# Performance work log

Hardware: AMD Instinct MI355X
Metric: run time of the kernel (lower is better)

The kernel has to match this reference:

```python
import jax, jax.numpy as jnp
import numpy as np

TARGET_MAIN_CONTRIBUTION = 0.6
CONTRIB_LOSS_COEF = 0.01
TOP_K = 2
NEG_INF = -1e9


def _gat(x, adj, W1, a1s, a1d, W2, a2s, a2d):
    """Dense 2-layer GAT (pyGAT style): multi-head concat + ELU, then one output head.
    x: [B,S,Fin], adj: [B,S,S], W1: [H,Fin,Fh], a1s/a1d: [H,Fh], W2: [H*Fh,Fout], a2s/a2d: [Fout]."""
    mask = adj > 0  # [B,S,S]
    h = jnp.einsum('bsf,hfo->bhso', x, W1)                      # [B,H,S,Fh]
    es = jnp.einsum('bhso,ho->bhs', h, a1s)
    ed = jnp.einsum('bhso,ho->bhs', h, a1d)
    e = jax.nn.leaky_relu(es[:, :, :, None] + ed[:, :, None, :], 0.2)  # [B,H,S,S]
    att = jax.nn.softmax(jnp.where(mask[:, None], e, NEG_INF), axis=-1)
    h1 = jax.nn.elu(jnp.einsum('bhst,bhto->bhso', att, h))      # [B,H,S,Fh]
    B, H, S, Fh = h1.shape
    h1 = h1.transpose(0, 2, 1, 3).reshape(B, S, H * Fh)         # concat heads
    h2 = h1 @ W2                                                # [B,S,Fout]
    e2 = jax.nn.leaky_relu((h2 @ a2s)[:, :, None] + (h2 @ a2d)[:, None, :], 0.2)
    att2 = jax.nn.softmax(jnp.where(mask, e2, NEG_INF), axis=-1)
    return jnp.einsum('bst,bto->bso', att2, h2)


def setup_inputs() -> dict:
    B, S, D, H, Hd, E = 4, 1024, 256, 6, 64, 3
    key = jax.random.key(0)
    ks = jax.random.split(key, 20)
    feature = jax.random.normal(ks[0], (B, S, D), dtype=jnp.float32)
    # sparse-ish binary adjacency with self-loops
    adj = (jax.random.uniform(ks[1], (B, S, S)) < 0.05).astype(jnp.float32)
    adj = jnp.maximum(adj, jnp.eye(S, dtype=jnp.float32)[None])
    p = lambda k, shape: jax.random.normal(k, shape, dtype=jnp.float32) * 0.1
    return {
        'feature': feature, 'adj': adj,
        'main_W1': p(ks[2], (H, D, Hd)), 'main_a1s': p(ks[3], (H, Hd)), 'main_a1d': p(ks[4], (H, Hd)),
        'main_W2': p(ks[5], (H * Hd, D)), 'main_a2s': p(ks[6], (D,)), 'main_a2d': p(ks[7], (D,)),
        'dep_W1': p(ks[8], (E, H, D, Hd)), 'dep_a1s': p(ks[9], (E, H, Hd)), 'dep_a1d': p(ks[10], (E, H, Hd)),
        'dep_W2': p(ks[11], (E, H * Hd, D)), 'dep_a2s': p(ks[12], (E, D)), 'dep_a2d': p(ks[13], (E, D)),
        'router_W': p(ks[14], (D, E)),
        'blend_W': p(ks[15], (D, D)), 'blend_b': jnp.zeros((D,), dtype=jnp.float32),
        'doc_num': 4, 'sect_num': 32,
    }


def reference(feature, adj, main_W1, main_a1s, main_a1d, main_W2, main_a2s, main_a2d,
              dep_W1, dep_a1s, dep_a1d, dep_W2, dep_a2s, dep_a2d,
              router_W, blend_W, blend_b, doc_num, sect_num):
    B, S, D = feature.shape
    E = router_W.shape[1]
    # main expert on full graph
    main_output = _gat(feature, adj, main_W1, main_a1s, main_a1d, main_W2, main_a2s, main_a2d)
    # per-expert adjacency views (zero out columns by node type)
    col = jnp.arange(S)
    sent_cols = (col < S - sect_num - doc_num).astype(adj.dtype)
    sect_cols = ((col >= S - sect_num - doc_num) & (col < S - doc_num)).astype(adj.dtype)
    doc_cols = (col >= S - doc_num).astype(adj.dtype)
    adj_stack = jnp.stack([adj * sent_cols, adj * sect_cols, adj * doc_cols])  # [E,B,S,S]
    # fixed top-k router
    x_flat = feature.reshape(-1, D)
    gate_probs = jax.nn.softmax(x_flat @ router_W, axis=-1)      # [B*S,E]
    _, top_idx = jax.lax.top_k(gate_probs, TOP_K)                # [B*S,k]
    routing_mask = jax.nn.one_hot(top_idx, E, dtype=feature.dtype).sum(axis=-2)  # [B*S,E] binary
    routing_mask = routing_mask.reshape(B, S, E)
    mask_e = routing_mask.transpose(2, 0, 1)[..., None]          # [E,B,S,1]
    # deputy experts: masked input, masked output, accumulate
    x_e = feature[None] * mask_e                                 # [E,B,S,D]
    dep_out = jax.vmap(_gat)(x_e, adj_stack, dep_W1, dep_a1s, dep_a1d, dep_W2, dep_a2s, dep_a2d)
    deputy_output = (dep_out * mask_e).sum(axis=0)               # [B,S,D]
    # blend gate
    blend_weight = jax.nn.sigmoid(feature @ blend_W + blend_b)
    final_output = blend_weight * main_output + (1.0 - blend_weight) * deputy_output
    main_contribution = blend_weight.mean()
    contribution_loss = jnp.abs(main_contribution - TARGET_MAIN_CONTRIBUTION) * CONTRIB_LOSS_COEF
    return final_output, contribution_loss, main_contribution
```

## Files before the change

kernel.cpp:

```cpp
#include <hip/hip_runtime.h>
#include <math.h>

#define B 4
#define S 1024
#define D 256
#define H 6
#define HD 64
#define NE 3
#define HHD 384
#define ROWS (B*S)
#define MAXN 128

typedef __attribute__((ext_vector_type(8))) short bf8_t;
typedef __attribute__((ext_vector_type(4))) float f32x4;

__device__ __forceinline__ float leaky(float x){ return x > 0.f ? x : 0.2f*x; }

__device__ __forceinline__ unsigned short f2bf(float f){
    union { float f; unsigned int u; } v; v.f = f;
    unsigned int u = v.u;
    return (unsigned short)((u + 0x7FFFu + ((u >> 16) & 1u)) >> 16);
}
__device__ __forceinline__ float bf2f(unsigned short h){
    union { unsigned int u; float f; } v; v.u = ((unsigned int)h) << 16;
    return v.f;
}
__device__ __forceinline__ float blo(unsigned int u){
    union { unsigned int u; float f; } v; v.u = u << 16; return v.f;
}
__device__ __forceinline__ float bhi(unsigned int u){
    union { unsigned int u; float f; } v; v.u = u & 0xffff0000u; return v.f;
}
__device__ __forceinline__ float i2f(int t){
    union { int i; float f; } v; v.i = t; return v.f;
}
__device__ __forceinline__ int f2i(float f){
    union { float f; int i; } v; v.f = f; return v.i;
}
__device__ __forceinline__ unsigned int pk2(float lo, float hi){
    return (unsigned)f2bf(lo) | ((unsigned)f2bf(hi) << 16);
}

struct P {
    const float *feature, *adj;
    const float *main_W1, *dep_W1, *main_W2, *dep_W2, *blend_W, *router_W;
    const int *doc_p, *sect_p;
    const float *main_a1s, *main_a1d, *dep_a1s, *dep_a1d;
    const float *main_a2s, *main_a2d, *dep_a2s, *dep_a2d;
    const float *blend_b;
    unsigned short *featbf; short *nbr; int4 *nbc;
    unsigned short *w1nk, *w2nk, *bwt;
    float *es8, *ed8, *gatebuf;
    unsigned short *htn4, *h2n4, *h1c4;
    float *f2s4, *f2d4, *meanV1p, *meanV2, *sumBuf, *rmask;
    float *outp;
};

#define PB_CONV   1024
#define PB_NBR    1024
#define PB_W1     1536
#define PB_W2     1536
#define PB_BW      256
#define PB_ZERO    177
#define PB_ROUTER 1024
#define PB_TOTAL  (PB_CONV + PB_NBR + PB_W1 + PB_W2 + PB_BW + PB_ZERO + PB_ROUTER)
#define NZERO     45088

__global__ __launch_bounds__(256) void prep_kernel(P pp)
{
    int blk = blockIdx.x, tid = threadIdx.x;
    if (blk < PB_CONV){
        int idx = blk*256 + tid;
        float4 v = ((const float4*)pp.feature)[idx];
        ushort4 o;
        o.x = f2bf(v.x); o.y = f2bf(v.y); o.z = f2bf(v.z); o.w = f2bf(v.w);
        ((ushort4*)pp.featbf)[idx] = o;
        return;
    }
    blk -= PB_CONV;
    if (blk < PB_NBR){
        int wave = tid >> 6, lane = tid & 63;
        int row = blk*4 + wave;
        int b1 = S - *pp.sect_p - *pp.doc_p;
        int b2 = S - *pp.doc_p;
        const float* ar = pp.adj + (size_t)row*S + lane*16;
        float a[16];
        #pragma unroll
        for (int q = 0; q < 4; q++){
            float4 v = ((const float4*)ar)[q];
            a[q*4+0] = v.x; a[q*4+1] = v.y; a[q*4+2] = v.z; a[q*4+3] = v.w;
        }
        int t0 = lane*16;
        int k = 0, c1 = 0, c2 = 0;
        #pragma unroll
        for (int i = 0; i < 16; i++){
            if (a[i] > 0.f){
                k++;
                int t = t0 + i;
                if (t < b1) c1++;
                if (t < b2) c2++;
            }
        }
        int inc = k;
        #pragma unroll
        for (int d = 1; d < 64; d <<= 1){
            int u = __shfl_up(inc, d);
            if (lane >= d) inc += u;
        }
        int off = inc - k;
        int total = __shfl(inc, 63);
        int o = row*MAXN + off;
        #pragma unroll
        for (int i = 0; i < 16; i++){
            if (a[i] > 0.f) pp.nbr[o++] = (short)(t0 + i);
        }
        for (int d = 32; d; d >>= 1){
            c1 += __shfl_down(c1, d);
            c2 += __shfl_down(c2, d);
        }
        if (lane == 0) pp.nbc[row] = make_int4(total, c1, c2, 0);
        return;
    }
    blk -= PB_NBR;
    if (blk < PB_W1){
        int e = blk / 384;
        int idx = (blk - e*384)*256 + tid;
        const float* src = (e == 0) ? pp.main_W1 : pp.dep_W1 + (size_t)(e-1)*H*D*HD;
        int n = idx >> 8, k = idx & 255;
        int h = n >> 6, o = n & 63;
        pp.w1nk[(size_t)e*HHD*D + idx] = f2bf(src[(h*D + k)*HD + o]);
        return;
    }
    blk -= PB_W1;
    if (blk < PB_W2){
        int g = blk*256 + tid;
        int e = g / (D*HHD);
        int rem = g - e*(D*HHD);
        int n = rem / HHD, k = rem - n*HHD;
        const float* src = (e == 0) ? pp.main_W2 : pp.dep_W2 + (size_t)(e-1)*HHD*D;
        pp.w2nk[g] = f2bf(src[k*D + n]);
        return;
    }
    blk -= PB_W2;
    if (blk < PB_BW){
        int col = blk, k = tid;
        pp.bwt[col*D + k] = f2bf(pp.blend_W[k*D + col]);
        return;
    }
    blk -= PB_BW;
    if (blk < PB_ZERO){
        int idx = blk*256 + tid;
        if (idx < NZERO) pp.f2s4[idx] = 0.f;
        return;
    }
    blk -= PB_ZERO;
    {
        int wave = tid >> 6, lane = tid & 63;
        int row = blk*4 + wave;
        float4 xv = ((const float4*)(pp.feature + (size_t)row*D))[lane];
        int f = lane*4;
        float xa[4] = {xv.x, xv.y, xv.z, xv.w};
        float p0 = 0.f, p1 = 0.f, p2 = 0.f;
        #pragma unroll
        for (int j = 0; j < 4; j++){
            p0 += xa[j]*pp.router_W[(f+j)*NE + 0];
            p1 += xa[j]*pp.router_W[(f+j)*NE + 1];
            p2 += xa[j]*pp.router_W[(f+j)*NE + 2];
        }
        for (int off = 32; off; off >>= 1){
            p0 += __shfl_down(p0, off);
            p1 += __shfl_down(p1, off);
            p2 += __shfl_down(p2, off);
        }
        if (lane == 0){
            float p[3] = {p0, p1, p2};
            int ex = 0;
            for (int e = 1; e < NE; e++) if (p[e] <= p[ex]) ex = e;
            for (int e = 0; e < NE; e++) pp.rmask[e*ROWS + row] = (e == ex) ? 0.f : 1.f;
        }
    }
}

__global__ __launch_bounds__(256, 4) void gemm1_kernel(P pp)
{
    __shared__ float ep[2][2][64][17];
    int tid = threadIdx.x, wave = tid >> 6, lane = tid & 63;
    int quad = lane >> 4, l16 = lane & 15;
    int e = blockIdx.z;
    int n0 = blockIdx.y*64;
    f32x4 z4 = {0.f,0.f,0.f,0.f};
    bf8_t bz = {0,0,0,0,0,0,0,0};

    if (e == 4){
        if (blockIdx.x >= 2) return;
        int m0 = blockIdx.x*128;
        const unsigned short* arow0 = pp.bwt + (size_t)(m0 + wave*16 + l16)*D + quad*8;
        const unsigned short* arow1 = arow0 + (size_t)64*D;
        const unsigned short* brow[4];
        #pragma unroll
        for (int j = 0; j < 4; j++)
            brow[j] = pp.featbf + (size_t)(n0 + j*16 + l16)*D + quad*8;
        f32x4 acc[8] = {z4, z4, z4, z4, z4, z4, z4, z4};
        bf8_t a0F = *(const bf8_t*)(arow0);
        bf8_t a1F = *(const bf8_t*)(arow1);
        bf8_t bF[4];
        #pragma unroll
        for (int j = 0; j < 4; j++) bF[j] = *(const bf8_t*)(brow[j]);
        #pragma unroll
        for (int it = 0; it < D/32; it++){
            bf8_t a0C = a0F, a1C = a1F;
            bf8_t bC[4] = {bF[0], bF[1], bF[2], bF[3]};
            if (it + 1 < D/32){
                int kn = (it + 1)*32;
                a0F = *(const bf8_t*)(arow0 + kn);
                a1F = *(const bf8_t*)(arow1 + kn);
                #pragma unroll
                for (int j = 0; j < 4; j++) bF[j] = *(const bf8_t*)(brow[j] + kn);
            }
            #pragma unroll
            for (int j = 0; j < 4; j++){
                acc[j]   = __builtin_amdgcn_mfma_f32_16x16x32_bf16(a0C, bC[j], acc[j],   0, 0, 0);
                acc[4+j] = __builtin_amdgcn_mfma_f32_16x16x32_bf16(a1C, bC[j], acc[4+j], 0, 0, 0);
            }
        }
        int mbase0 = m0 + wave*16 + quad*4;
        int mbase1 = mbase0 + 64;
        float bias0[4], bias1[4];
        #pragma unroll
        for (int r = 0; r < 4; r++){ bias0[r] = pp.blend_b[mbase0 + r]; bias1[r] = pp.blend_b[mbase1 + r]; }
        float lsum = 0.f;
        #pragma unroll
        for (int j = 0; j < 4; j++){
            int rown = n0 + j*16 + l16;
            f32x4 st0, st1;
            #pragma unroll
            for (int r = 0; r < 4; r++){
                float g0 = 1.f/(1.f + __expf(-(acc[j][r] + bias0[r])));
                float g1 = 1.f/(1.f + __expf(-(acc[4+j][r] + bias1[r])));
                lsum += g0 + g1;
                st0[r] = g0; st1[r] = g1;
            }
            *(f32x4*)(pp.gatebuf + (size_t)rown*D + mbase0) = st0;
            *(f32x4*)(pp.gatebuf + (size_t)rown*D + mbase1) = st1;
        }
        float* redp = &ep[0][0][0][0];
        redp[tid] = lsum;
        __syncthreads();
        for (int sft = 128; sft; sft >>= 1){
            if (tid < sft) redp[tid] += redp[tid + sft];
            __syncthreads();
        }
        if (tid == 0) atomicAdd(pp.sumBuf, redp[0]);
        return;
    }

    int p = blockIdx.x;
    int m0 = p*128;
    const unsigned short* arow0 = pp.w1nk + (size_t)e*HHD*D + (size_t)(m0 + wave*16 + l16)*D + quad*8;
    const unsigned short* arow1 = arow0 + (size_t)64*D;
    const unsigned short* brow[4];
    bool zr[4];
    #pragma unroll
    for (int j = 0; j < 4; j++){
        int n = n0 + j*16 + l16;
        brow[j] = pp.featbf + (size_t)n*D + quad*8;
        zr[j] = (e > 0) ? (pp.rmask[(size_t)(e-1)*ROWS + n] == 0.f) : false;
    }
    f32x4 acc[8] = {z4, z4, z4, z4, z4, z4, z4, z4};
    bf8_t a0F = *(const bf8_t*)(arow0);
    bf8_t a1F = *(const bf8_t*)(arow1);
    bf8_t bF[4];
    #pragma unroll
    for (int j = 0; j < 4; j++) bF[j] = zr[j] ? bz : *(const bf8_t*)(brow[j]);
    #pragma unroll
    for (int it = 0; it < D/32; it++){
        bf8_t a0C = a0F, a1C = a1F;
        bf8_t bC[4] = {bF[0], bF[1], bF[2], bF[3]};
        if (it + 1 < D/32){
            int kn = (it + 1)*32;
            a0F = *(const bf8_t*)(arow0 + kn);
            a1F = *(const bf8_t*)(arow1 + kn);
            #pragma unroll
            for (int j = 0; j < 4; j++) bF[j] = zr[j] ? bz : *(const bf8_t*)(brow[j] + kn);
        }
        #pragma unroll
        for (int j = 0; j < 4; j++){
            acc[j]   = __builtin_amdgcn_mfma_f32_16x16x32_bf16(a0C, bC[j], acc[j],   0, 0, 0);
            acc[4+j] = __builtin_amdgcn_mfma_f32_16x16x32_bf16(a1C, bC[j], acc[4+j], 0, 0, 0);
        }
    }
    int b = n0 >> 10;
    int mbase0 = m0 + wave*16 + quad*4;
    int mbase1 = mbase0 + 64;
    int obase = wave*16 + quad*4;
    int h0 = p*2, h1 = p*2 + 1;
    unsigned int* hp4 = (unsigned int*)pp.htn4;
    #pragma unroll
    for (int j = 0; j < 4; j++){
        int row = n0 + j*16 + l16;
        unsigned int* dst = hp4 + ((size_t)e*ROWS + row)*256 + obase*4 + p;
        dst[0]  = pk2(acc[j][0], acc[4+j][0]);
        dst[4]  = pk2(acc[j][1], acc[4+j][1]);
        dst[8]  = pk2(acc[j][2], acc[4+j][2]);
        dst[12] = pk2(acc[j][3], acc[4+j][3]);
    }
    const float* a1sp = (e == 0) ? pp.main_a1s : pp.dep_a1s + (size_t)(e-1)*H*HD;
    const float* a1dp = (e == 0) ? pp.main_a1d : pp.dep_a1d + (size_t)(e-1)*H*HD;
    float s0v[4], d0v[4], s1v[4], d1v[4];
    #pragma unroll
    for (int r = 0; r < 4; r++){
        s0v[r] = a1sp[mbase0 + r]; d0v[r] = a1dp[mbase0 + r];
        s1v[r] = a1sp[mbase1 + r]; d1v[r] = a1dp[mbase1 + r];
    }
    #pragma unroll
    for (int j = 0; j < 4; j++){
        float ps0 = 0.f, pd0 = 0.f, ps1 = 0.f, pd1 = 0.f;
        #pragma unroll
        for (int r = 0; r < 4; r++){
            ps0 += acc[j][r]*s0v[r];   pd0 += acc[j][r]*d0v[r];
            ps1 += acc[4+j][r]*s1v[r]; pd1 += acc[4+j][r]*d1v[r];
        }
        ep[0][0][j*16 + l16][wave*4 + quad] = ps0;
        ep[0][1][j*16 + l16][wave*4 + quad] = pd0;
        ep[1][0][j*16 + l16][wave*4 + quad] = ps1;
        ep[1][1][j*16 + l16][wave*4 + quad] = pd1;
    }
    float* mvb = pp.meanV1p + ((size_t)e*B + b)*512;
    #pragma unroll
    for (int r = 0; r < 4; r++){
        float cm0 = acc[0][r] + acc[1][r] + acc[2][r] + acc[3][r];
        float cm1 = acc[4][r] + acc[5][r] + acc[6][r] + acc[7][r];
        for (int off = 8; off; off >>= 1){
            cm0 += __shfl_down(cm0, off, 16);
            cm1 += __shfl_down(cm1, off, 16);
        }
        if (l16 == 0){
            atomicAdd(mvb + (obase + r)*8 + h0, cm0*(1.f/(float)S));
            atomicAdd(mvb + (obase + r)*8 + h1, cm1*(1.f/(float)S));
        }
    }
    __syncthreads();
    {
        int hh = tid >> 7, arr = (tid >> 6) & 1, sl = tid & 63;
        float sum = 0.f;
        #pragma unroll
        for (int i = 0; i < 16; i++) sum += ep[hh][arr][sl][i];
        int n = n0 + sl;
        float* dst = arr ? pp.ed8 : pp.es8;
        dst[(((size_t)e*B + (n >> 10))*S + (n & 1023))*8 + (p*2 + hh)] = sum;
    }
}

__global__ __launch_bounds__(256) void a1_kernel(P pp)
{
    __shared__ f32x4 wMa[MAXN], wMb[MAXN], wDa[MAXN], wDb[MAXN];
    __shared__ f32x4 paccA[4][64], paccB[4][64];
    __shared__ float pdenM[2][6];
    __shared__ float pdenD[2][3][6];
    int tid = threadIdx.x, wave = tid >> 6, lane = tid & 63;
    int s = blockIdx.x, b = blockIdx.y;
    int row = b*S + s;
    int4 c = pp.nbc[row];
    const short* nl = pp.nbr + (size_t)row*MAXN;

    if (wave < 2){
        const float* esp = pp.es8 + ((size_t)b*S + s)*8;
        f32x4 eslo = *(const f32x4*)esp;
        f32x4 eshi = *(const f32x4*)(esp + 4);
        float esv[6] = {eslo[0], eslo[1], eslo[2], eslo[3], eshi[0], eshi[1]};
        const float* edb = pp.ed8 + (size_t)b*S*8;
        int i = wave*64 + lane;
        float w[6] = {0,0,0,0,0,0};
        if (i < c.x){
            int t = nl[i];
            const float* epn = edb + (size_t)t*8;
            f32x4 d0 = *(const f32x4*)epn;
            f32x4 d1 = *(const f32x4*)(epn + 4);
            float edv[6] = {d0[0], d0[1], d0[2], d0[3], d1[0], d1[1]};
            #pragma unroll
            for (int h = 0; h < 6; h++) w[h] = __expf(leaky(esv[h] + edv[h]));
            f32x4 ra = {w[0], w[1], w[2], w[3]};
            f32x4 rb = {w[4], w[5], i2f(t), 0.f};
            wMa[i] = ra; wMb[i] = rb;
        }
        #pragma unroll
        for (int h = 0; h < 6; h++){
            float x = w[h];
            for (int o2 = 32; o2; o2 >>= 1) x += __shfl_down(x, o2);
            if (lane == 0) pdenM[wave][h] = x;
        }
    } else {
        int i = (wave - 2)*64 + lane;
        int tg = (i < c.y) ? 1 : ((i < c.z) ? 2 : 3);
        float w[6] = {0,0,0,0,0,0};
        if (i < c.x){
            int t = nl[i];
            const float* esp = pp.es8 + (((size_t)tg*B + b)*S + s)*8;
            f32x4 eslo = *(const f32x4*)esp;
            f32x4 eshi = *(const f32x4*)(esp + 4);
            const float* epn = pp.ed8 + (((size_t)tg*B + b)*S + (size_t)t)*8;
            f32x4 d0 = *(const f32x4*)epn;
            f32x4 d1 = *(const f32x4*)(epn + 4);
            float es6[6] = {eslo[0], eslo[1], eslo[2], eslo[3], eshi[0], eshi[1]};
            float ed6[6] = {d0[0], d0[1], d0[2], d0[3], d1[0], d1[1]};
            #pragma unroll
            for (int h = 0; h < 6; h++) w[h] = __expf(leaky(es6[h] + ed6[h]));
            float zf = (pp.rmask[(size_t)(tg-1)*ROWS + (size_t)b*S + t] == 0.f) ? 1.f : 0.f;
            f32x4 ra = {w[0], w[1], w[2], w[3]};
            f32x4 rb = {w[4], w[5], zf, 0.f};
            wDa[i] = ra; wDb[i] = rb;
        }
        #pragma unroll
        for (int g = 1; g <= 3; g++){
            #pragma unroll
            for (int h = 0; h < 6; h++){
                float x = (tg == g) ? w[h] : 0.f;
                for (int o2 = 32; o2; o2 >>= 1) x += __shfl_down(x, o2);
                if (lane == 0) pdenD[wave-2][g-1][h] = x;
            }
        }
    }
    __syncthreads();

    const unsigned int* V0 = (const unsigned int*)pp.htn4 + (size_t)b*S*256;
    float accM[6] = {0,0,0,0,0,0};
    int rlo[3] = {0, c.y, c.z};
    int rhi[3] = {c.y, c.z, c.x};
    for (int rg = 0; rg < 3; rg++){
        const unsigned int* Ve = (const unsigned int*)pp.htn4 + ((size_t)(rg+1)*ROWS + (size_t)b*S)*256;
        float accD[6] = {0,0,0,0,0,0};
        #pragma unroll 2
        for (int j = rlo[rg] + wave; j < rhi[rg]; j += 4){
            f32x4 ma = wMa[j], mb = wMb[j];
            f32x4 da = wDa[j], db = wDb[j];
            int t = f2i(mb[2]);
            uint4 vm = *(const uint4*)(V0 + ((size_t)t*64 + lane)*4);
            accM[0] += ma[0]*blo(vm.x); accM[1] += ma[1]*bhi(vm.x);
            accM[2] += ma[2]*blo(vm.y); accM[3] += ma[3]*bhi(vm.y);
            accM[4] += mb[0]*blo(vm.z); accM[5] += mb[1]*bhi(vm.z);
            if (db[2] == 0.f){
                uint4 vd = *(const uint4*)(Ve + ((size_t)t*64 + lane)*4);
                accD[0] += da[0]*blo(vd.x); accD[1] += da[1]*bhi(vd.x);
                accD[2] += da[2]*blo(vd.y); accD[3] += da[3]*bhi(vd.y);
                accD[4] += db[0]*blo(vd.z); accD[5] += db[1]*bhi(vd.z);
            }
        }
        {
            f32x4 pa = {accD[0], accD[1], accD[2], accD[3]};
            f32x4 pb = {accD[4], accD[5], 0.f, 0.f};
            paccA[wave][lane] = pa; paccB[wave][lane] = pb;
        }
        __syncthreads();
        if (wave == 0){
            unsigned short* outp = pp.h1c4 + ((size_t)(rg+1)*ROWS + row)*HHD;
            bool has = rhi[rg] > rlo[rg];
            const float* mv = pp.meanV1p + ((size_t)(rg+1)*B + b)*512 + lane*8;
            f32x4 q0 = paccA[0][lane], q1 = paccA[1][lane], q2 = paccA[2][lane], q3 = paccA[3][lane];
            f32x4 r0 = paccB[0][lane], r1 = paccB[1][lane], r2 = paccB[2][lane], r3 = paccB[3][lane];
            float sum6[6];
            sum6[0] = q0[0]+q1[0]+q2[0]+q3[0];
            sum6[1] = q0[1]+q1[1]+q2[1]+q3[1];
            sum6[2] = q0[2]+q1[2]+q2[2]+q3[2];
            sum6[3] = q0[3]+q1[3]+q2[3]+q3[3];
            sum6[4] = r0[0]+r1[0]+r2[0]+r3[0];
            sum6[5] = r0[1]+r1[1]+r2[1]+r3[1];
            #pragma unroll
            for (int h = 0; h < 6; h++){
                float den = pdenD[0][rg][h] + pdenD[1][rg][h];
                float v = has ? sum6[h]/den : mv[h];
                v = v > 0.f ? v : __expf(v) - 1.f;
                outp[h*64 + lane] = f2bf(v);
            }
        }
        __syncthreads();
    }
    {
        f32x4 pa = {accM[0], accM[1], accM[2], accM[3]};
        f32x4 pb = {accM[4], accM[5], 0.f, 0.f};
        paccA[wave][lane] = pa; paccB[wave][lane] = pb;
    }
    __syncthreads();
    if (wave == 0){
        unsigned short* outp = pp.h1c4 + (size_t)row*HHD;
        f32x4 q0 = paccA[0][lane], q1 = paccA[1][lane], q2 = paccA[2][lane], q3 = paccA[3][lane];
        f32x4 r0 = paccB[0][lane], r1 = paccB[1][lane], r2 = paccB[2][lane], r3 = paccB[3][lane];
        float sum6[6];
        sum6[0] = q0[0]+q1[0]+q2[0]+q3[0];
        sum6[1] = q0[1]+q1[1]+q2[1]+q3[1];
        sum6[2] = q0[2]+q1[2]+q2[2]+q3[2];
        sum6[3] = q0[3]+q1[3]+q2[3]+q3[3];
        sum6[4] = r0[0]+r1[0]+r2[0]+r3[0];
        sum6[5] = r0[1]+r1[1]+r2[1]+r3[1];
        #pragma unroll
        for (int h = 0; h < 6; h++){
            float den = pdenM[0][h] + pdenM[1][h];
            float v = sum6[h]/den;
            v = v > 0.f ? v : __expf(v) - 1.f;
            outp[h*64 + lane] = f2bf(v);
        }
    }
}

__global__ __launch_bounds__(256, 4) void gemm2_kernel(P pp)
{
    __shared__ float ep[2][2][64][17];
    int tid = threadIdx.x, wave = tid >> 6, lane = tid & 63;
    int quad = lane >> 4, l16 = lane & 15;
    int e = blockIdx.z;
    int m0 = blockIdx.x*128;
    int n0 = blockIdx.y*64;
    f32x4 z4 = {0.f,0.f,0.f,0.f};
    const unsigned short* arow0 = pp.w2nk + (size_t)e*D*HHD + (size_t)(m0 + wave*16 + l16)*HHD + quad*8;
    const unsigned short* arow1 = arow0 + (size_t)64*HHD;
    const unsigned short* brow[4];
    #pragma unroll
    for (int j = 0; j < 4; j++)
        brow[j] = pp.h1c4 + (size_t)e*ROWS*HHD + (size_t)(n0 + j*16 + l16)*HHD + quad*8;
    f32x4 acc[8] = {z4, z4, z4, z4, z4, z4, z4, z4};
    bf8_t a0F = *(const bf8_t*)(arow0);
    bf8_t a1F = *(const bf8_t*)(arow1);
    bf8_t bF[4];
    #pragma unroll
    for (int j = 0; j < 4; j++) bF[j] = *(const bf8_t*)(brow[j]);
    #pragma unroll
    for (int it = 0; it < HHD/32; it++){
        bf8_t a0C = a0F, a1C = a1F;
        bf8_t bC[4] = {bF[0], bF[1], bF[2], bF[3]};
        if (it + 1 < HHD/32){
            int kn = (it + 1)*32;
            a0F = *(const bf8_t*)(arow0 + kn);
            a1F = *(const bf8_t*)(arow1 + kn);
            #pragma unroll
            for (int j = 0; j < 4; j++) bF[j] = *(const bf8_t*)(brow[j] + kn);
        }
        #pragma unroll
        for (int j = 0; j < 4; j++){
            acc[j]   = __builtin_amdgcn_mfma_f32_16x16x32_bf16(a0C, bC[j], acc[j],   0, 0, 0);
            acc[4+j] = __builtin_amdgcn_mfma_f32_16x16x32_bf16(a1C, bC[j], acc[4+j], 0, 0, 0);
        }
    }
    int b = n0 >> 10;
    int mbase0 = m0 + wave*16 + quad*4;
    int mbase1 = mbase0 + 64;
    #pragma unroll
    for (int j = 0; j < 4; j++){
        int row = n0 + j*16 + l16;
        ushort4 o0, o1;
        o0.x = f2bf(acc[j][0]);   o0.y = f2bf(acc[j][1]);
        o0.z = f2bf(acc[j][2]);   o0.w = f2bf(acc[j][3]);
        o1.x = f2bf(acc[4+j][0]); o1.y = f2bf(acc[4+j][1]);
        o1.z = f2bf(acc[4+j][2]); o1.w = f2bf(acc[4+j][3]);
        *(ushort4*)(pp.h2n4 + ((size_t)e*ROWS + row)*D + mbase0) = o0;
        *(ushort4*)(pp.h2n4 + ((size_t)e*ROWS + row)*D + mbase1) = o1;
    }
    const float* a2sp = (e == 0) ? pp.main_a2s : pp.dep_a2s + (size_t)(e-1)*D;
    const float* a2dp = (e == 0) ? pp.main_a2d : pp.dep_a2d + (size_t)(e-1)*D;
    float s0v[4], d0v[4], s1v[4], d1v[4];
    #pragma unroll
    for (int r = 0; r < 4; r++){
        s0v[r] = a2sp[mbase0 + r]; d0v[r] = a2dp[mbase0 + r];
        s1v[r] = a2sp[mbase1 + r]; d1v[r] = a2dp[mbase1 + r];
    }
    #pragma unroll
    for (int j = 0; j < 4; j++){
        float ps0 = 0.f, pd0 = 0.f, ps1 = 0.f, pd1 = 0.f;
        #pragma unroll
        for (int r = 0; r < 4; r++){
            ps0 += acc[j][r]*s0v[r];   pd0 += acc[j][r]*d0v[r];
            ps1 += acc[4+j][r]*s1v[r]; pd1 += acc[4+j][r]*d1v[r];
        }
        ep[0][0][j*16 + l16][wave*4 + quad] = ps0;
        ep[0][1][j*16 + l16][wave*4 + quad] = pd0;
        ep[1][0][j*16 + l16][wave*4 + quad] = ps1;
        ep[1][1][j*16 + l16][wave*4 + quad] = pd1;
    }
    #pragma unroll
    for (int r = 0; r < 4; r++){
        float cm0 = acc[0][r] + acc[1][r] + acc[2][r] + acc[3][r];
        float cm1 = acc[4][r] + acc[5][r] + acc[6][r] + acc[7][r];
        for (int off = 8; off; off >>= 1){
            cm0 += __shfl_down(cm0, off, 16);
            cm1 += __shfl_down(cm1, off, 16);
        }
        if (l16 == 0){
            atomicAdd(pp.meanV2 + ((size_t)e*B + b)*D + mbase0 + r, cm0*(1.f/(float)S));
            atomicAdd(pp.meanV2 + ((size_t)e*B + b)*D + mbase1 + r, cm1*(1.f/(float)S));
        }
    }
    __syncthreads();
    {
        int hh = tid >> 7, arr = (tid >> 6) & 1, sl = tid & 63;
        float sum = 0.f;
        #pragma unroll
        for (int i = 0; i < 16; i++) sum += ep[hh][arr][sl][i];
        int n = n0 + sl;
        float* dst = arr ? pp.f2d4 : pp.f2s4;
        atomicAdd(dst + (size_t)e*ROWS + n, sum);
    }
}

__global__ __launch_bounds__(256) void a2_kernel(P pp)
{
    __shared__ float2 wrec0[MAXN];
    __shared__ float2 wrec1[MAXN];
    __shared__ float pacc[3][256];
    __shared__ float pden[4][4];
    int tid = threadIdx.x;
    int wave = tid >> 6, lane = tid & 63;
    int s = blockIdx.x, b = blockIdx.y;
    int row = b*S + s;
    int4 c = pp.nbc[row];
    float rm0 = pp.rmask[row], rm1 = pp.rmask[ROWS + row], rm2 = pp.rmask[2*ROWS + row];
    const short* nl = pp.nbr + (size_t)row*MAXN;
    if (wave < 2){
        int i = wave*64 + lane;
        float w = 0.f;
        if (i < c.x){
            int t = nl[i];
            float fs = pp.f2s4[row];
            w = __expf(leaky(fs + pp.f2d4[(size_t)b*S + t]));
            float2 r; r.x = w; r.y = i2f(t);
            wrec0[i] = r;
        }
        float dsum = w;
        for (int o2 = 32; o2; o2 >>= 1) dsum += __shfl_down(dsum, o2);
        if (lane == 0) pden[wave][0] = dsum;
    } else {
        int i = (wave - 2)*64 + lane;
        float w = 0.f, d1 = 0.f, d2 = 0.f, d3 = 0.f;
        if (i < c.x){
            int t = nl[i];
            int tag = (i < c.y) ? 1 : ((i < c.z) ? 2 : 3);
            float act = (tag == 1) ? rm0 : ((tag == 2) ? rm1 : rm2);
            if (act != 0.f){
                float fs = pp.f2s4[(size_t)tag*ROWS + row];
                w = __expf(leaky(fs + pp.f2d4[(size_t)tag*ROWS + (size_t)b*S + t]));
            }
            float2 r; r.x = w; r.y = i2f(t);
            wrec1[i] = r;
            if (tag == 1) d1 = w; else if (tag == 2) d2 = w; else d3 = w;
        }
        for (int o2 = 32; o2; o2 >>= 1){
            d1 += __shfl_down(d1, o2);
            d2 += __shfl_down(d2, o2);
            d3 += __shfl_down(d3, o2);
        }
        if (lane == 0){ pden[wave][1] = d1; pden[wave][2] = d2; pden[wave][3] = d3; }
    }
    __syncthreads();
    float acc[4] = {0.f, 0.f, 0.f, 0.f};
    if (wave < 2){
        float inv = 1.f/(pden[0][0] + pden[1][0]);
        const unsigned short* V = pp.h2n4 + (size_t)b*S*D;
        #pragma unroll 4
        for (int j = wave; j < c.x; j += 2){
            float2 r = wrec0[j];
            float wv = r.x*inv;
            int t = f2i(r.y);
            const unsigned short* vp = V + (size_t)t*D + lane*4;
            uint2 dv = *(const uint2*)vp;
            acc[0] += wv*blo(dv.x); acc[1] += wv*bhi(dv.x);
            acc[2] += wv*blo(dv.y); acc[3] += wv*bhi(dv.y);
        }
    } else {
        int rlo[3] = {0, c.y, c.z};
        int rhi[3] = {c.y, c.z, c.x};
        float ract[3] = {rm0, rm1, rm2};
        for (int rg = 0; rg < 3; rg++){
            if (ract[rg] == 0.f || rhi[rg] <= rlo[rg]) continue;
            float inv = 1.f/(pden[2][rg+1] + pden[3][rg+1]);
            const unsigned short* V = pp.h2n4 + ((size_t)(rg+1)*ROWS + (size_t)b*S)*D;
            #pragma unroll 4
            for (int j = rlo[rg] + (wave - 2); j < rhi[rg]; j += 2){
                float2 r = wrec1[j];
                float wv = r.x*inv;
                int t = f2i(r.y);
                const unsigned short* vp = V + (size_t)t*D + lane*4;
                uint2 dv = *(const uint2*)vp;
                acc[0] += wv*blo(dv.x); acc[1] += wv*bhi(dv.x);
                acc[2] += wv*blo(dv.y); acc[3] += wv*bhi(dv.y);
            }
        }
    }
    if (wave >= 1){
        #pragma unroll
        for (int q = 0; q < 4; q++) pacc[wave-1][lane*4 + q] = acc[q];
    }
    __syncthreads();
    if (wave == 0){
        float4 g4 = *(const float4*)(pp.gatebuf + (size_t)row*D + lane*4);
        float dep_mv[4] = {0.f, 0.f, 0.f, 0.f};
        if (rm0 != 0.f && c.y == 0){
            float4 mv = *(const float4*)(pp.meanV2 + ((size_t)1*B + b)*D + lane*4);
            dep_mv[0] += mv.x; dep_mv[1] += mv.y; dep_mv[2] += mv.z; dep_mv[3] += mv.w;
        }
        if (rm1 != 0.f && c.z == c.y){
            float4 mv = *(const float4*)(pp.meanV2 + ((size_t)2*B + b)*D + lane*4);
            dep_mv[0] += mv.x; dep_mv[1] += mv.y; dep_mv[2] += mv.z; dep_mv[3] += mv.w;
        }
        if (rm2 != 0.f && c.x == c.z){
            float4 mv = *(const float4*)(pp.meanV2 + ((size_t)3*B + b)*D + lane*4);
            dep_mv[0] += mv.x; dep_mv[1] += mv.y; dep_mv[2] += mv.z; dep_mv[3] += mv.w;
        }
        float g[4] = {g4.x, g4.y, g4.z, g4.w};
        float4 o;
        float* op = &o.x;
        #pragma unroll
        for (int q = 0; q < 4; q++){
            int col = lane*4 + q;
            float a0 = acc[q] + pacc[0][col];
            float dep = pacc[1][col] + pacc[2][col] + dep_mv[q];
            op[q] = g[q]*a0 + (1.f - g[q])*dep;
        }
        *(float4*)(pp.outp + (size_t)row*D + lane*4) = o;
    }
    if (blockIdx.x == 0 && blockIdx.y == 0 && tid == 0){
        float mc = pp.sumBuf[0] / (float)(ROWS*D);
        pp.outp[ROWS*D]     = fabsf(mc - 0.6f)*0.01f;
        pp.outp[ROWS*D + 1] = mc;
    }
}

extern "C" void kernel_launch(void* const* d_in, const int* in_sizes, int n_in,
                              void* d_out, int out_size, void* d_ws, size_t ws_size,
                              hipStream_t stream)
{
    P hp;
    hp.feature  = (const float*)d_in[0];
    hp.adj      = (const float*)d_in[1];
    hp.main_W1  = (const float*)d_in[2];
    hp.main_a1s = (const float*)d_in[3];
    hp.main_a1d = (const float*)d_in[4];
    hp.main_W2  = (const float*)d_in[5];
    hp.main_a2s = (const float*)d_in[6];
    hp.main_a2d = (const float*)d_in[7];
    hp.dep_W1   = (const float*)d_in[8];
    hp.dep_a1s  = (const float*)d_in[9];
    hp.dep_a1d  = (const float*)d_in[10];
    hp.dep_W2   = (const float*)d_in[11];
    hp.dep_a2s  = (const float*)d_in[12];
    hp.dep_a2d  = (const float*)d_in[13];
    hp.router_W = (const float*)d_in[14];
    hp.blend_W  = (const float*)d_in[15];
    hp.blend_b  = (const float*)d_in[16];
    hp.doc_p    = (const int*)d_in[17];
    hp.sect_p   = (const int*)d_in[18];

    char* ws = (char*)d_ws;
    size_t off = 0;
    hp.featbf = (unsigned short*)(ws + off); off += (size_t)ROWS*D*2;
    hp.nbr    = (short*)(ws + off);          off += (size_t)ROWS*MAXN*2;
    hp.nbc    = (int4*)(ws + off);           off += (size_t)ROWS*16;
    hp.w1nk   = (unsigned short*)(ws + off); off += (size_t)4*HHD*D*2;
    hp.w2nk   = (unsigned short*)(ws + off); off += (size_t)4*D*HHD*2;
    hp.bwt    = (unsigned short*)(ws + off); off += (size_t)D*D*2;
    hp.es8 = (float*)(ws + off); off += (size_t)4*B*S*8*4;
    hp.ed8 = (float*)(ws + off); off += (size_t)4*B*S*8*4;
    hp.gatebuf = (float*)(ws + off); off += (size_t)ROWS*D*4;
    hp.htn4 = (unsigned short*)(ws + off); off += (size_t)4*ROWS*256*4;
    hp.h2n4 = (unsigned short*)(ws + off); off += (size_t)4*ROWS*D*2;
    hp.h1c4 = (unsigned short*)(ws + off); off += (size_t)4*ROWS*HHD*2;
    hp.f2s4    = (float*)(ws + off); off += (size_t)4*ROWS*4;
    hp.f2d4    = (float*)(ws + off); off += (size_t)4*ROWS*4;
    hp.meanV1p = (float*)(ws + off); off += (size_t)4*B*512*4;
    hp.meanV2  = (float*)(ws + off); off += (size_t)4*B*D*4;
    hp.sumBuf  = (float*)(ws + off); off += 128;
    hp.rmask   = (float*)(ws + off); off += (size_t)NE*ROWS*4;
    hp.outp    = (float*)d_out;

    prep_kernel<<<PB_TOTAL, 256, 0, stream>>>(hp);
    gemm1_kernel<<<dim3(3, ROWS/64, 5), 256, 0, stream>>>(hp);
    a1_kernel<<<dim3(S, B), 256, 0, stream>>>(hp);
    gemm2_kernel<<<dim3(D/128, ROWS/64, 4), 256, 0, stream>>>(hp);
    a2_kernel<<<dim3(S, B), 256, 0, stream>>>(hp);
}
```

Baseline: 226.0 us.

## Store layer-1 head features as per-pair planes via LDS-staged coalesced writes

The interleaved htn4 buffer, which held 4 uint slots per output with one unused, is replaced by three separate planes per expert, one per head pair. gemm1 now stages the packed bf16 results in shared memory and writes each plane with coalesced 16-byte stores. The a1 gather now reads three 4-byte words from separate planes instead of one 16-byte word. This drops the wasted padding slot and the strided scatter stores, but each gathered neighbour now costs three memory transactions instead of one.

Result: faster. 221.5 us (-2.0%).

```diff
diff --git a/kernel.cpp b/kernel.cpp
--- a/kernel.cpp
+++ b/kernel.cpp
@@ -10,6 +10,7 @@
 #define HHD 384
 #define ROWS (B*S)
 #define MAXN 128
+#define PLN ((size_t)ROWS*64)
 
 typedef __attribute__((ext_vector_type(8))) short bf8_t;
 typedef __attribute__((ext_vector_type(4))) float f32x4;
@@ -51,7 +52,8 @@
     unsigned short *featbf; short *nbr; int4 *nbc;
     unsigned short *w1nk, *w2nk, *bwt;
     float *es8, *ed8, *gatebuf;
-    unsigned short *htn4, *h2n4, *h1c4;
+    unsigned int *htp;
+    unsigned short *h2n4, *h1c4;
     float *f2s4, *f2d4, *meanV1p, *meanV2, *sumBuf, *rmask;
     float *outp;
 };
@@ -183,7 +185,9 @@
 
 __global__ __launch_bounds__(256, 4) void gemm1_kernel(P pp)
 {
-    __shared__ float ep[2][2][64][17];
+    __shared__ __align__(16) char smem[17408];
+    float (*ep)[2][64][17] = (float (*)[2][64][17])smem;
+    unsigned int (*tile)[68] = (unsigned int (*)[68])smem;
     int tid = threadIdx.x, wave = tid >> 6, lane = tid & 63;
     int quad = lane >> 4, l16 = lane & 15;
     int e = blockIdx.z;
@@ -243,7 +247,7 @@
             *(f32x4*)(pp.gatebuf + (size_t)rown*D + mbase0) = st0;
             *(f32x4*)(pp.gatebuf + (size_t)rown*D + mbase1) = st1;
         }
-        float* redp = &ep[0][0][0][0];
+        float* redp = (float*)smem;
         redp[tid] = lsum;
         __syncthreads();
         for (int sft = 128; sft; sft >>= 1){
@@ -294,16 +298,6 @@
     int mbase1 = mbase0 + 64;
     int obase = wave*16 + quad*4;
     int h0 = p*2, h1 = p*2 + 1;
-    unsigned int* hp4 = (unsigned int*)pp.htn4;
-    #pragma unroll
-    for (int j = 0; j < 4; j++){
-        int row = n0 + j*16 + l16;
-        unsigned int* dst = hp4 + ((size_t)e*ROWS + row)*256 + obase*4 + p;
-        dst[0]  = pk2(acc[j][0], acc[4+j][0]);
-        dst[4]  = pk2(acc[j][1], acc[4+j][1]);
-        dst[8]  = pk2(acc[j][2], acc[4+j][2]);
-        dst[12] = pk2(acc[j][3], acc[4+j][3]);
-    }
     const float* a1sp = (e == 0) ? pp.main_a1s : pp.dep_a1s + (size_t)(e-1)*H*HD;
     const float* a1dp = (e == 0) ? pp.main_a1d : pp.dep_a1d + (size_t)(e-1)*H*HD;
     float s0v[4], d0v[4], s1v[4], d1v[4];
@@ -348,6 +342,27 @@
         int n = n0 + sl;
         float* dst = arr ? pp.ed8 : pp.es8;
         dst[(((size_t)e*B + (n >> 10))*S + (n & 1023))*8 + (p*2 + hh)] = sum;
+    }
+    __syncthreads();
+    #pragma unroll
+    for (int j = 0; j < 4; j++){
+        int rloc = j*16 + l16;
+        tile[rloc][obase + 0] = pk2(acc[j][0], acc[4+j][0]);
+        tile[rloc][obase + 1] = pk2(acc[j][1], acc[4+j][1]);
+        tile[rloc][obase + 2] = pk2(acc[j][2], acc[4+j][2]);
+        tile[rloc][obase + 3] = pk2(acc[j][3], acc[4+j][3]);
+    }
+    __syncthreads();
+    {
+        unsigned int* plane = pp.htp + (size_t)(e*3 + p)*PLN;
+        int o4 = (tid & 15)*4;
+        int rsub = tid >> 4;
+        #pragma unroll
+        for (int pass = 0; pass < 4; pass++){
+            int rloc = pass*16 + rsub;
+            uint4 v = *(const uint4*)&tile[rloc][o4];
+            *(uint4*)(plane + (size_t)(n0 + rloc)*64 + o4) = v;
+        }
     }
 }
 
@@ -422,27 +437,31 @@
     }
     __syncthreads();
 
-    const unsigned int* V0 = (const unsigned int*)pp.htn4 + (size_t)b*S*256;
+    const unsigned int* Vm = pp.htp + (size_t)b*S*64 + lane;
     float accM[6] = {0,0,0,0,0,0};
     int rlo[3] = {0, c.y, c.z};
     int rhi[3] = {c.y, c.z, c.x};
     for (int rg = 0; rg < 3; rg++){
-        const unsigned int* Ve = (const unsigned int*)pp.htn4 + ((size_t)(rg+1)*ROWS + (size_t)b*S)*256;
+        const unsigned int* Vd = pp.htp + (size_t)(rg+1)*3*PLN + (size_t)b*S*64 + lane;
         float accD[6] = {0,0,0,0,0,0};
         #pragma unroll 2
         for (int j = rlo[rg] + wave; j < rhi[rg]; j += 4){
             f32x4 ma = wMa[j], mb = wMb[j];
             f32x4 da = wDa[j], db = wDb[j];
-            int t = f2i(mb[2]);
-            uint4 vm = *(const uint4*)(V0 + ((size_t)t*64 + lane)*4);
-            accM[0] += ma[0]*blo(vm.x); accM[1] += ma[1]*bhi(vm.x);
-            accM[2] += ma[2]*blo(vm.y); accM[3] += ma[3]*bhi(vm.y);
-            accM[4] += mb[0]*blo(vm.z); accM[5] += mb[1]*bhi(vm.z);
+            size_t toff = (size_t)f2i(mb[2])*64;
+            unsigned int u0 = Vm[toff];
+            unsigned int u1 = Vm[toff + PLN];
+            unsigned int u2 = Vm[toff + 2*PLN];
+            accM[0] += ma[0]*blo(u0); accM[1] += ma[1]*bhi(u0);
+            accM[2] += ma[2]*blo(u1); accM[3] += ma[3]*bhi(u1);
+            accM[4] += mb[0]*blo(u2); accM[5] += mb[1]*bhi(u2);
             if (db[2] == 0.f){
-                uint4 vd = *(const uint4*)(Ve + ((size_t)t*64 + lane)*4);
-                accD[0] += da[0]*blo(vd.x); accD[1] += da[1]*bhi(vd.x);
-                accD[2] += da[2]*blo(vd.y); accD[3] += da[3]*bhi(vd.y);
-                accD[4] += db[0]*blo(vd.z); accD[5] += db[1]*bhi(vd.z);
+                unsigned int d0 = Vd[toff];
+                unsigned int d1 = Vd[toff + PLN];
+                unsigned int d2 = Vd[toff + 2*PLN];
+                accD[0] += da[0]*blo(d0); accD[1] += da[1]*bhi(d0);
+                accD[2] += da[2]*blo(d1); accD[3] += da[3]*bhi(d1);
+                accD[4] += db[0]*blo(d2); accD[5] += db[1]*bhi(d2);
             }
         }
         {
@@ -757,7 +776,7 @@
     hp.es8 = (float*)(ws + off); off += (size_t)4*B*S*8*4;
     hp.ed8 = (float*)(ws + off); off += (size_t)4*B*S*8*4;
     hp.gatebuf = (float*)(ws + off); off += (size_t)ROWS*D*4;
-    hp.htn4 = (unsigned short*)(ws + off); off += (size_t)4*ROWS*256*4;
+    hp.htp  = (unsigned int*)(ws + off);     off += (size_t)12*PLN*4;
     hp.h2n4 = (unsigned short*)(ws + off); off += (size_t)4*ROWS*D*2;
     hp.h1c4 = (unsigned short*)(ws + off); off += (size_t)4*ROWS*HHD*2;
     hp.f2s4    = (float*)(ws + off); off += (size_t)4*ROWS*4;
```
